# Optimization experiments

Measured on AMD Instinct MI355X. Metric: run time of the kernel, lower is better.

## Reference

```python
import jax, jax.numpy as jnp
import numpy as np

H = 4        # no_heads
CH = 32      # per-head hidden (c_hidden)
INF = 1.0e9

def setup_inputs() -> dict:
    key = jax.random.key(0)
    ks = jax.random.split(key, 8)
    B, I, J, C = 1, 256, 256, 128
    s = 0.02
    return {
        "x": jax.random.normal(ks[0], (B, I, J, C), jnp.float32),
        "mask": jnp.ones((B, I, J), jnp.float32),
        "chunk_size": 0,
        "ln_w": jnp.ones((C,), jnp.float32),
        "ln_b": jnp.zeros((C,), jnp.float32),
        "w_tri": jax.random.normal(ks[1], (C, H), jnp.float32) * s,
        "wq": jax.random.normal(ks[2], (C, H * CH), jnp.float32) * s,
        "wk": jax.random.normal(ks[3], (C, H * CH), jnp.float32) * s,
        "wv": jax.random.normal(ks[4], (C, H * CH), jnp.float32) * s,
        "wg": jax.random.normal(ks[5], (C, H * CH), jnp.float32) * s,
        "bg": jnp.zeros((H * CH,), jnp.float32),
        "wo": jax.random.normal(ks[6], (H * CH, C), jnp.float32) * s,
        "bo": jnp.zeros((C,), jnp.float32),
    }

def _layer_norm(x, w, b, eps=1e-5):
    mu = jnp.mean(x, axis=-1, keepdims=True)
    var = jnp.mean(jnp.square(x - mu), axis=-1, keepdims=True)
    return (x - mu) * jax.lax.rsqrt(var + eps) * w + b

def reference(x, mask, chunk_size, ln_w, ln_b, w_tri, wq, wk, wv, wg, bg, wo, bo):
    # starting=True -> no transpose of (I, J)
    B, I, J, C = x.shape
    xn = _layer_norm(x, ln_w, ln_b)                                   # [B,I,J,C]
    # biases
    mask_bias = (INF * (mask - 1.0))[:, :, None, None, :]             # [B,I,1,1,J]
    tri_bias = jnp.einsum("bijc,ch->bhij", xn, w_tri)[:, None]        # [B,1,H,I,J]
    # gated multi-head attention over the J axis (per row I)
    q = (xn @ wq).reshape(B, I, J, H, CH) * (CH ** -0.5)              # [B,I,J,H,CH]
    k = (xn @ wk).reshape(B, I, J, H, CH)
    v = (xn @ wv).reshape(B, I, J, H, CH)
    scores = jnp.einsum("biqhd,bikhd->bihqk", q, k) + mask_bias + tri_bias
    a = jax.nn.softmax(scores, axis=-1)                               # [B,I,H,J,J]
    o = jnp.einsum("bihqk,bikhd->biqhd", a, v)                        # [B,I,J,H,CH]
    g = jax.nn.sigmoid(xn @ wg + bg).reshape(B, I, J, H, CH)
    o = (o * g).reshape(B, I, J, H * CH)
    return o @ wo + bo                                                # [B,I,J,C]
```

## Files before the change

### kernel.cpp

```cpp
#include <hip/hip_runtime.h>
#include <math.h>

#define NI 256
#define NJ 256
#define NC 128
#define NH 4
#define NCH 32

typedef __attribute__((ext_vector_type(8)))  __bf16        bf16x8;
typedef __attribute__((ext_vector_type(8)))  unsigned short u16x8;
typedef __attribute__((ext_vector_type(4)))  unsigned int   u32x4;
typedef __attribute__((ext_vector_type(16))) float         f32x16;

__device__ __forceinline__ unsigned short f2bf(float f) {
    unsigned u = __builtin_bit_cast(unsigned, f);
    u += 0x7fffu + ((u >> 16) & 1u);
    return (unsigned short)(u >> 16);
}
__device__ __forceinline__ float bf2f(unsigned short s) {
    return __builtin_bit_cast(float, ((unsigned)s) << 16);
}
__device__ __forceinline__ f32x16 fzero16() {
    f32x16 z;
#pragma unroll
    for (int r = 0; r < 16; ++r) z[r] = 0.f;
    return z;
}
__device__ __forceinline__ f32x16 mfma16(bf16x8 a, bf16x8 b, f32x16 c) {
    return __builtin_amdgcn_mfma_f32_32x32x16_bf16(a, b, c, 0, 0, 0);
}

__global__ __launch_bounds__(256) void convert_weights(
    const float* __restrict__ wq, const float* __restrict__ wk,
    const float* __restrict__ wv, const float* __restrict__ wg,
    const float* __restrict__ wo, const float* __restrict__ w_tri,
    unsigned short* __restrict__ Wt_all, unsigned short* __restrict__ Wto,
    unsigned short* __restrict__ Wtri_pad)
{
    int id = blockIdx.x * 256 + threadIdx.x;
    if (id < 4 * 16384) {
        int m = id >> 14, r = id & 16383;
        int kk = r >> 7, c = r & 127;
        const float* W = (m == 0) ? wq : (m == 1) ? wk : (m == 2) ? wv : wg;
        Wt_all[(m * 128 + c) * 128 + kk] = f2bf(W[kk * 128 + c]);
    } else if (id < 5 * 16384) {
        int r = id - 4 * 16384;
        int kk = r >> 7, c = r & 127;
        Wto[c * 128 + kk] = f2bf(wo[kk * 128 + c]);
    } else {
        int r = id - 5 * 16384;
        int col = r >> 7, kk = r & 127;
        Wtri_pad[col * 128 + kk] = (col < NH) ? f2bf(w_tri[kk * NH + col]) : (unsigned short)0;
    }
}

#define XNP 136
__global__ __launch_bounds__(256, 2) void ln_proj_mfma(
    const float* __restrict__ x, const float* __restrict__ ln_w, const float* __restrict__ ln_b,
    const unsigned short* __restrict__ Wt_all, const unsigned short* __restrict__ Wtri_pad,
    const float* __restrict__ bg,
    unsigned short* __restrict__ q, unsigned short* __restrict__ k,
    unsigned short* __restrict__ v, unsigned short* __restrict__ g,
    float* __restrict__ tri)
{
    __shared__ unsigned short xn[64 * XNP];
    const int tid = threadIdx.x;
    const long tok0 = (long)blockIdx.x * 64;

    const int lane8 = tid & 7;
#pragma unroll
    for (int p = 0; p < 2; ++p) {
        const int t = p * 32 + (tid >> 3);
        const float4* xrow = (const float4*)(x + (tok0 + t) * NC + lane8 * 16);
        float4 xv[4];
        float s = 0.f;
#pragma unroll
        for (int u = 0; u < 4; ++u) {
            xv[u] = xrow[u];
            s += xv[u].x + xv[u].y + xv[u].z + xv[u].w;
        }
#pragma unroll
        for (int off = 4; off; off >>= 1) s += __shfl_down(s, off, 8);
        const float mu = __shfl(s, 0, 8) * (1.f / (float)NC);
        float s2 = 0.f;
#pragma unroll
        for (int u = 0; u < 4; ++u) {
            float dx;
            dx = xv[u].x - mu; s2 += dx * dx;
            dx = xv[u].y - mu; s2 += dx * dx;
            dx = xv[u].z - mu; s2 += dx * dx;
            dx = xv[u].w - mu; s2 += dx * dx;
        }
#pragma unroll
        for (int off = 4; off; off >>= 1) s2 += __shfl_down(s2, off, 8);
        const float rstd = rsqrtf(__shfl(s2, 0, 8) * (1.f / (float)NC) + 1e-5f);
#pragma unroll
        for (int u = 0; u < 4; ++u) {
            const int c = lane8 * 16 + u * 4;
            const float4 lw = *(const float4*)(ln_w + c);
            const float4 lb = *(const float4*)(ln_b + c);
            float o0 = (xv[u].x - mu) * rstd * lw.x + lb.x;
            float o1 = (xv[u].y - mu) * rstd * lw.y + lb.y;
            float o2 = (xv[u].z - mu) * rstd * lw.z + lb.z;
            float o3 = (xv[u].w - mu) * rstd * lw.w + lb.w;
            unsigned p0 = (unsigned)f2bf(o0) | ((unsigned)f2bf(o1) << 16);
            unsigned p1 = (unsigned)f2bf(o2) | ((unsigned)f2bf(o3) << 16);
            *(unsigned*)&xn[t * XNP + c]     = p0;
            *(unsigned*)&xn[t * XNP + c + 2] = p1;
        }
    }
    __syncthreads();

    const int w = tid >> 6, L = tid & 63, lh = L >> 5, lc = L & 31;
    f32x16 acc[2][4], accT[2];
#pragma unroll
    for (int mt = 0; mt < 2; ++mt) {
        accT[mt] = fzero16();
#pragma unroll
        for (int nt = 0; nt < 4; ++nt) acc[mt][nt] = fzero16();
    }

#pragma unroll
    for (int k0 = 0; k0 < 8; ++k0) {
        bf16x8 a0 = *(const bf16x8*)&xn[(lc)      * XNP + k0 * 16 + lh * 8];
        bf16x8 a1 = *(const bf16x8*)&xn[(32 + lc) * XNP + k0 * 16 + lh * 8];
#pragma unroll
        for (int nt = 0; nt < 4; ++nt) {
            const int ntile = w + 4 * nt;
            bf16x8 b = *(const bf16x8*)&Wt_all[(ntile * 32 + lc) * 128 + k0 * 16 + lh * 8];
            acc[0][nt] = mfma16(a0, b, acc[0][nt]);
            acc[1][nt] = mfma16(a1, b, acc[1][nt]);
        }
        bf16x8 bt = *(const bf16x8*)&Wtri_pad[lc * 128 + k0 * 16 + lh * 8];
        accT[0] = mfma16(a0, bt, accT[0]);
        accT[1] = mfma16(a1, bt, accT[1]);
    }

    const int a_row = (int)(tok0 >> 8);
    const int b0    = (int)(tok0 & 255);
    int rowl[16];
#pragma unroll
    for (int r = 0; r < 16; ++r) rowl[r] = (r & 3) + 8 * (r >> 2) + 4 * lh;

    const float bgv = bg[w * 32 + lc];
#pragma unroll
    for (int nt = 0; nt < 4; ++nt) {
        unsigned short* O = (nt == 0) ? q : (nt == 1) ? k : (nt == 2) ? v : g;
        unsigned short* Ob = O + (((long)a_row * NH + w) * NJ + b0) * NCH + lc;
#pragma unroll
        for (int mt = 0; mt < 2; ++mt) {
#pragma unroll
            for (int r = 0; r < 16; ++r) {
                const int row = mt * 32 + rowl[r];
                float val = acc[mt][nt][r];
                if (nt == 0) val *= 0.17677669529663689f;
                if (nt == 3) val = __builtin_amdgcn_rcpf(1.f + __expf(-(val + bgv)));
                Ob[(long)row * NCH] = f2bf(val);
            }
        }
    }
    if (lc < NH) {
        float* tb = tri + ((long)lc * NI + a_row) * NJ + b0;
#pragma unroll
        for (int mt = 0; mt < 2; ++mt)
#pragma unroll
            for (int r = 0; r < 16; ++r)
                tb[mt * 32 + rowl[r]] = accT[mt][r];
    }
}

#define LSP 260
__global__ __launch_bounds__(256) void swizzle_triT(
    const float* __restrict__ tri, float* __restrict__ tswz)
{
    __shared__ float Ls[32 * LSP];
    const int h = blockIdx.x, qt = blockIdx.y;
    const int tid = threadIdx.x;
#pragma unroll
    for (int it = 0; it < 8; ++it) {
        const int fi = it * 256 + tid;
        const int row = fi >> 6, c4 = fi & 63;
        *(float4*)&Ls[row * LSP + c4 * 4] =
            *(const float4*)(tri + ((long)h * NI + qt * 32 + row) * NJ + c4 * 4);
    }
    __syncthreads();
    const int kt = tid >> 5;
    const int lane2 = (tid & 31) * 2;
    float* dst = tswz + (((long)(h * 8 + qt) * 8 + kt) * 64 + lane2) * 16;
#pragma unroll
    for (int sub = 0; sub < 2; ++sub) {
        const int lane = lane2 + sub;
        const int lc = lane & 31, lhh = lane >> 5;
        float vals[16];
#pragma unroll
        for (int r = 0; r < 16; ++r)
            vals[r] = Ls[lc * LSP + kt * 32 + (r & 3) + 8 * (r >> 2) + 4 * lhh];
#pragma unroll
        for (int u = 0; u < 4; ++u)
            *(float4*)(dst + sub * 16 + u * 4) =
                make_float4(vals[4*u], vals[4*u+1], vals[4*u+2], vals[4*u+3]);
    }
}

#define KSP 40
#define VTP 264
#define GSP 40
#define OSP 36
__global__ __launch_bounds__(256, 2) void attn_fused(
    const unsigned short* __restrict__ q, const unsigned short* __restrict__ k,
    const unsigned short* __restrict__ v, const unsigned short* __restrict__ g,
    const float* __restrict__ tswz, const float* __restrict__ mask,
    const unsigned short* __restrict__ Wto, const float* __restrict__ bo,
    float* __restrict__ out)
{
    __shared__ char smem[48640];
    unsigned short* Ks = (unsigned short*)smem;
    unsigned short* Vt = (unsigned short*)(smem + 20480);
    unsigned short* Gs = (unsigned short*)(smem + 37376);
    float*       maskb = (float*)(smem + 47616);
    float*        outs = (float*)smem;

    const int i = blockIdx.x, qh = blockIdx.y;
    const int tid = threadIdx.x;
    const int w = tid >> 6, L = tid & 63, lh = L >> 5, lc = L & 31;
    const int qt = qh * 4 + w;
    const int qrow = qt * 32 + lc;

    maskb[tid] = 1.0e9f * (mask[i * NJ + tid] - 1.0f);

    f32x16 outacc[4];
#pragma unroll
    for (int ct = 0; ct < 4; ++ct) outacc[ct] = fzero16();

    for (int h = 0; h < NH; ++h) {
        if (h) __syncthreads();
        const long base = ((long)i * NH + h) * NJ * NCH;

#pragma unroll
        for (int it = 0; it < 4; ++it) {
            const int idx = it * 256 + tid;
            const int key = idx >> 2, c8 = (idx & 3) * 8;
            *(bf16x8*)&Ks[key * KSP + c8] = *(const bf16x8*)(k + base + key * NCH + c8);
        }
        {
            const int key = tid;
            const u16x8 r0 = *(const u16x8*)(v + base + key * NCH);
            const u16x8 r1 = *(const u16x8*)(v + base + key * NCH + 8);
            const u16x8 r2 = *(const u16x8*)(v + base + key * NCH + 16);
            const u16x8 r3 = *(const u16x8*)(v + base + key * NCH + 24);
#pragma unroll
            for (int u = 0; u < 8; ++u) {
                Vt[(u)      * VTP + key] = r0[u];
                Vt[(u + 8)  * VTP + key] = r1[u];
                Vt[(u + 16) * VTP + key] = r2[u];
                Vt[(u + 24) * VTP + key] = r3[u];
            }
        }
#pragma unroll
        for (int it = 0; it < 2; ++it) {
            const int idx = it * 256 + tid;
            const int row = idx >> 2, c8 = (idx & 3) * 8;
            *(bf16x8*)&Gs[row * GSP + c8] =
                *(const bf16x8*)(g + base + (qh * 128 + row) * NCH + c8);
        }
        __syncthreads();

        const bf16x8 a0 = *(const bf16x8*)(q + base + (long)qrow * NCH + lh * 8);
        const bf16x8 a1 = *(const bf16x8*)(q + base + (long)qrow * NCH + 16 + lh * 8);
        const float* tbase = tswz + ((long)(h * 8 + qt) * 8) * 1024 + (long)L * 16;

        float ls = 0.f;
        f32x16 O = fzero16();

#pragma unroll
        for (int t = 0; t < 8; ++t) {
            bf16x8 kb0 = *(const bf16x8*)&Ks[(t * 32 + lc) * KSP + lh * 8];
            bf16x8 kb1 = *(const bf16x8*)&Ks[(t * 32 + lc) * KSP + 16 + lh * 8];
            f32x16 s = fzero16();
            s = mfma16(kb0, a0, s);
            s = mfma16(kb1, a1, s);

            unsigned pk[8];
            const float* tv = tbase + (long)t * 1024;
#pragma unroll
            for (int gg = 0; gg < 4; ++gg) {
                const float4 tb = *(const float4*)(tv + gg * 4);
                const float4 mb = *(const float4*)&maskb[t * 32 + gg * 8 + 4 * lh];
                const float p0 = __expf(fminf(s[4 * gg + 0] + tb.x + mb.x, 30.f));
                const float p1 = __expf(fminf(s[4 * gg + 1] + tb.y + mb.y, 30.f));
                const float p2 = __expf(fminf(s[4 * gg + 2] + tb.z + mb.z, 30.f));
                const float p3 = __expf(fminf(s[4 * gg + 3] + tb.w + mb.w, 30.f));
                ls += (p0 + p1) + (p2 + p3);
                pk[2 * gg]     = (unsigned)f2bf(p0) | ((unsigned)f2bf(p1) << 16);
                pk[2 * gg + 1] = (unsigned)f2bf(p2) | ((unsigned)f2bf(p3) << 16);
            }

#pragma unroll
            for (int ss = 0; ss < 2; ++ss) {
                const unsigned give0 = lh ? pk[4 * ss]     : pk[4 * ss + 2];
                const unsigned give1 = lh ? pk[4 * ss + 1] : pk[4 * ss + 3];
                const unsigned t0 = __shfl_xor(give0, 32);
                const unsigned t1 = __shfl_xor(give1, 32);
                u32x4 bw;
                bw[0] = lh ? t0 : pk[4 * ss];
                bw[1] = lh ? t1 : pk[4 * ss + 1];
                bw[2] = lh ? pk[4 * ss + 2] : t0;
                bw[3] = lh ? pk[4 * ss + 3] : t1;
                const bf16x8 pb = __builtin_bit_cast(bf16x8, bw);
                const bf16x8 va = *(const bf16x8*)&Vt[lc * VTP + t * 32 + ss * 16 + lh * 8];
                O = mfma16(va, pb, O);
            }
        }

        ls += __shfl_xor(ls, 32);
        const float rl = __builtin_amdgcn_rcpf(ls);
        unsigned pk2[8];
#pragma unroll
        for (int gg = 0; gg < 4; ++gg) {
            const ushort4 gv = *(const ushort4*)&Gs[(w * 32 + lc) * GSP + gg * 8 + 4 * lh];
            const float o0 = O[4 * gg + 0] * rl * bf2f(gv.x);
            const float o1 = O[4 * gg + 1] * rl * bf2f(gv.y);
            const float o2 = O[4 * gg + 2] * rl * bf2f(gv.z);
            const float o3 = O[4 * gg + 3] * rl * bf2f(gv.w);
            pk2[2 * gg]     = (unsigned)f2bf(o0) | ((unsigned)f2bf(o1) << 16);
            pk2[2 * gg + 1] = (unsigned)f2bf(o2) | ((unsigned)f2bf(o3) << 16);
        }

#pragma unroll
        for (int ss = 0; ss < 2; ++ss) {
            const unsigned give0 = lh ? pk2[4 * ss]     : pk2[4 * ss + 2];
            const unsigned give1 = lh ? pk2[4 * ss + 1] : pk2[4 * ss + 3];
            const unsigned t0 = __shfl_xor(give0, 32);
            const unsigned t1 = __shfl_xor(give1, 32);
            u32x4 bw;
            bw[0] = lh ? t0 : pk2[4 * ss];
            bw[1] = lh ? t1 : pk2[4 * ss + 1];
            bw[2] = lh ? pk2[4 * ss + 2] : t0;
            bw[3] = lh ? pk2[4 * ss + 3] : t1;
            const bf16x8 ogb = __builtin_bit_cast(bf16x8, bw);
#pragma unroll
            for (int ct = 0; ct < 4; ++ct) {
                const bf16x8 wa = *(const bf16x8*)&Wto[(ct * 32 + lc) * 128 + h * 32 + ss * 16 + lh * 8];
                outacc[ct] = mfma16(wa, ogb, outacc[ct]);
            }
        }
    }

    int rowl[16];
#pragma unroll
    for (int r = 0; r < 16; ++r) rowl[r] = (r & 3) + 8 * (r >> 2) + 4 * lh;
#pragma unroll
    for (int ct = 0; ct < 4; ++ct) {
        __syncthreads();
#pragma unroll
        for (int r = 0; r < 16; ++r)
            outs[(w * 32 + lc) * OSP + rowl[r]] = outacc[ct][r];
        __syncthreads();
#pragma unroll
        for (int it = 0; it < 4; ++it) {
            const int fi = it * 256 + tid;
            const int row = fi >> 3, c4 = fi & 7;
            const float4 vv = *(const float4*)&outs[row * OSP + c4 * 4];
            const float4 bo4 = *(const float4*)(bo + ct * 32 + c4 * 4);
            float4 st;
            st.x = vv.x + bo4.x; st.y = vv.y + bo4.y;
            st.z = vv.z + bo4.z; st.w = vv.w + bo4.w;
            *(float4*)(out + ((long)i * NJ + qh * 128 + row) * NC + ct * 32 + c4 * 4) = st;
        }
    }
}

extern "C" void kernel_launch(void* const* d_in, const int* in_sizes, int n_in,
                              void* d_out, int out_size, void* d_ws, size_t ws_size,
                              hipStream_t stream) {
    const float* x     = (const float*)d_in[0];
    const float* mask  = (const float*)d_in[1];
    const float* ln_w  = (const float*)d_in[3];
    const float* ln_b  = (const float*)d_in[4];
    const float* w_tri = (const float*)d_in[5];
    const float* wq    = (const float*)d_in[6];
    const float* wk    = (const float*)d_in[7];
    const float* wv    = (const float*)d_in[8];
    const float* wg    = (const float*)d_in[9];
    const float* bg    = (const float*)d_in[10];
    const float* wo    = (const float*)d_in[11];
    const float* bo    = (const float*)d_in[12];
    float* out = (float*)d_out;

    char* p = (char*)d_ws;
    const long TOK = (long)NI * NJ;
    const long QB  = TOK * NC * sizeof(unsigned short);
    unsigned short* q  = (unsigned short*)p; p += QB;
    unsigned short* k  = (unsigned short*)p; p += QB;
    unsigned short* v  = (unsigned short*)p; p += QB;
    unsigned short* g  = (unsigned short*)p; p += QB;
    float* tri  = (float*)p; p += (long)NH * NI * NJ * sizeof(float);
    float* tswz = (float*)p; p += (long)NH * NI * NJ * sizeof(float);
    unsigned short* Wt_all   = (unsigned short*)p; p += 4 * 128 * 128 * sizeof(unsigned short);
    unsigned short* Wto      = (unsigned short*)p; p += 128 * 128 * sizeof(unsigned short);
    unsigned short* Wtri_pad = (unsigned short*)p; p += 32 * 128 * sizeof(unsigned short);

    hipLaunchKernelGGL(convert_weights, dim3(336), dim3(256), 0, stream,
                       wq, wk, wv, wg, wo, w_tri, Wt_all, Wto, Wtri_pad);
    hipLaunchKernelGGL(ln_proj_mfma, dim3(TOK / 64), dim3(256), 0, stream,
                       x, ln_w, ln_b, Wt_all, Wtri_pad, bg, q, k, v, g, tri);
    hipLaunchKernelGGL(swizzle_triT, dim3(NH, 8), dim3(256), 0, stream, tri, tswz);
    hipLaunchKernelGGL(attn_fused, dim3(NI, 2), dim3(256), 0, stream,
                       q, k, v, g, tswz, mask, Wto, bo, out);
}
```

Measured before the change: 179.8 us.

## Switch to fp16 MFMA, exp2 softmax, split keys across 8 waves, coalesce projection stores

Replaces bf16 with fp16 MFMA and round-toward-zero packing. Folds log2e into the scores, triangle bias and mask so softmax can use exp2, and loads the triangle bias straight into the accumulator. The attention kernel grows to 512 threads, with two waves per query tile each handling half the keys and merging partial results through LDS. The output projection is split across waves. The projection kernel stages outputs through LDS for vectorized stores, and the tri swizzle is retiled into smaller blocks. Trade-offs are fp16 range and precision and extra synchronization for the merge.

```diff
diff --git a/kernel.cpp b/kernel.cpp
--- a/kernel.cpp
+++ b/kernel.cpp
@@ -6,19 +6,18 @@
 #define NC 128
 #define NH 4
 #define NCH 32
-
-typedef __attribute__((ext_vector_type(8)))  __bf16        bf16x8;
-typedef __attribute__((ext_vector_type(8)))  unsigned short u16x8;
-typedef __attribute__((ext_vector_type(4)))  unsigned int   u32x4;
-typedef __attribute__((ext_vector_type(16))) float         f32x16;
-
-__device__ __forceinline__ unsigned short f2bf(float f) {
-    unsigned u = __builtin_bit_cast(unsigned, f);
-    u += 0x7fffu + ((u >> 16) & 1u);
-    return (unsigned short)(u >> 16);
-}
-__device__ __forceinline__ float bf2f(unsigned short s) {
-    return __builtin_bit_cast(float, ((unsigned)s) << 16);
+#define LOG2E 1.4426950408889634f
+
+typedef _Float16 f16x8 __attribute__((ext_vector_type(8)));
+typedef unsigned short u16x8 __attribute__((ext_vector_type(8)));
+typedef unsigned int u32x4 __attribute__((ext_vector_type(4)));
+typedef float f32x16 __attribute__((ext_vector_type(16)));
+
+__device__ __forceinline__ unsigned short f2h(float f) {
+    return __builtin_bit_cast(unsigned short, (_Float16)f);
+}
+__device__ __forceinline__ unsigned pkrtz(float a, float b) {
+    return __builtin_bit_cast(unsigned, __builtin_amdgcn_cvt_pkrtz(a, b));
 }
 __device__ __forceinline__ f32x16 fzero16() {
     f32x16 z;
@@ -26,8 +25,8 @@
     for (int r = 0; r < 16; ++r) z[r] = 0.f;
     return z;
 }
-__device__ __forceinline__ f32x16 mfma16(bf16x8 a, bf16x8 b, f32x16 c) {
-    return __builtin_amdgcn_mfma_f32_32x32x16_bf16(a, b, c, 0, 0, 0);
+__device__ __forceinline__ f32x16 mfma16f(f16x8 a, f16x8 b, f32x16 c) {
+    return __builtin_amdgcn_mfma_f32_32x32x16_f16(a, b, c, 0, 0, 0);
 }
 
 __global__ __launch_bounds__(256) void convert_weights(
@@ -42,15 +41,15 @@
         int m = id >> 14, r = id & 16383;
         int kk = r >> 7, c = r & 127;
         const float* W = (m == 0) ? wq : (m == 1) ? wk : (m == 2) ? wv : wg;
-        Wt_all[(m * 128 + c) * 128 + kk] = f2bf(W[kk * 128 + c]);
+        Wt_all[(m * 128 + c) * 128 + kk] = f2h(W[kk * 128 + c]);
     } else if (id < 5 * 16384) {
         int r = id - 4 * 16384;
         int kk = r >> 7, c = r & 127;
-        Wto[c * 128 + kk] = f2bf(wo[kk * 128 + c]);
+        Wto[c * 128 + kk] = f2h(wo[kk * 128 + c]);
     } else {
         int r = id - 5 * 16384;
         int col = r >> 7, kk = r & 127;
-        Wtri_pad[col * 128 + kk] = (col < NH) ? f2bf(w_tri[kk * NH + col]) : (unsigned short)0;
+        Wtri_pad[col * 128 + kk] = (col < NH) ? f2h(w_tri[kk * NH + col]) : (unsigned short)0;
     }
 }
 
@@ -103,10 +102,8 @@
             float o1 = (xv[u].y - mu) * rstd * lw.y + lb.y;
             float o2 = (xv[u].z - mu) * rstd * lw.z + lb.z;
             float o3 = (xv[u].w - mu) * rstd * lw.w + lb.w;
-            unsigned p0 = (unsigned)f2bf(o0) | ((unsigned)f2bf(o1) << 16);
-            unsigned p1 = (unsigned)f2bf(o2) | ((unsigned)f2bf(o3) << 16);
-            *(unsigned*)&xn[t * XNP + c]     = p0;
-            *(unsigned*)&xn[t * XNP + c + 2] = p1;
+            *(unsigned*)&xn[t * XNP + c]     = pkrtz(o0, o1);
+            *(unsigned*)&xn[t * XNP + c + 2] = pkrtz(o2, o3);
         }
     }
     __syncthreads();
@@ -122,18 +119,18 @@
 
 #pragma unroll
     for (int k0 = 0; k0 < 8; ++k0) {
-        bf16x8 a0 = *(const bf16x8*)&xn[(lc)      * XNP + k0 * 16 + lh * 8];
-        bf16x8 a1 = *(const bf16x8*)&xn[(32 + lc) * XNP + k0 * 16 + lh * 8];
+        f16x8 a0 = *(const f16x8*)&xn[(lc)      * XNP + k0 * 16 + lh * 8];
+        f16x8 a1 = *(const f16x8*)&xn[(32 + lc) * XNP + k0 * 16 + lh * 8];
 #pragma unroll
         for (int nt = 0; nt < 4; ++nt) {
             const int ntile = w + 4 * nt;
-            bf16x8 b = *(const bf16x8*)&Wt_all[(ntile * 32 + lc) * 128 + k0 * 16 + lh * 8];
-            acc[0][nt] = mfma16(a0, b, acc[0][nt]);
-            acc[1][nt] = mfma16(a1, b, acc[1][nt]);
-        }
-        bf16x8 bt = *(const bf16x8*)&Wtri_pad[lc * 128 + k0 * 16 + lh * 8];
-        accT[0] = mfma16(a0, bt, accT[0]);
-        accT[1] = mfma16(a1, bt, accT[1]);
+            f16x8 b = *(const f16x8*)&Wt_all[(ntile * 32 + lc) * 128 + k0 * 16 + lh * 8];
+            acc[0][nt] = mfma16f(a0, b, acc[0][nt]);
+            acc[1][nt] = mfma16f(a1, b, acc[1][nt]);
+        }
+        f16x8 bt = *(const f16x8*)&Wtri_pad[lc * 128 + k0 * 16 + lh * 8];
+        accT[0] = mfma16f(a0, bt, accT[0]);
+        accT[1] = mfma16f(a1, bt, accT[1]);
     }
 
     const int a_row = (int)(tok0 >> 8);
@@ -142,230 +139,261 @@
 #pragma unroll
     for (int r = 0; r < 16; ++r) rowl[r] = (r & 3) + 8 * (r >> 2) + 4 * lh;
 
+    if (lc < NH) {
+        float* tb = tri + ((long)lc * NI + a_row) * NJ + b0;
+#pragma unroll
+        for (int mt = 0; mt < 2; ++mt)
+#pragma unroll
+            for (int r = 0; r < 16; ++r)
+                tb[mt * 32 + rowl[r]] = accT[mt][r];
+    }
+
     const float bgv = bg[w * 32 + lc];
-#pragma unroll
-    for (int nt = 0; nt < 4; ++nt) {
-        unsigned short* O = (nt == 0) ? q : (nt == 1) ? k : (nt == 2) ? v : g;
-        unsigned short* Ob = O + (((long)a_row * NH + w) * NJ + b0) * NCH + lc;
+    const int token = tid >> 2, c8 = (tid & 3) * 8;
+#pragma unroll
+    for (int m = 0; m < 4; ++m) {
+        __syncthreads();
 #pragma unroll
         for (int mt = 0; mt < 2; ++mt) {
 #pragma unroll
             for (int r = 0; r < 16; ++r) {
                 const int row = mt * 32 + rowl[r];
-                float val = acc[mt][nt][r];
-                if (nt == 0) val *= 0.17677669529663689f;
-                if (nt == 3) val = __builtin_amdgcn_rcpf(1.f + __expf(-(val + bgv)));
-                Ob[(long)row * NCH] = f2bf(val);
-            }
-        }
-    }
-    if (lc < NH) {
-        float* tb = tri + ((long)lc * NI + a_row) * NJ + b0;
-#pragma unroll
-        for (int mt = 0; mt < 2; ++mt)
-#pragma unroll
-            for (int r = 0; r < 16; ++r)
-                tb[mt * 32 + rowl[r]] = accT[mt][r];
-    }
-}
-
-#define LSP 260
-__global__ __launch_bounds__(256) void swizzle_triT(
+                float val = acc[mt][m][r];
+                if (m == 0) val *= 0.25503486f;
+                if (m == 3) val = __builtin_amdgcn_rcpf(1.f + __builtin_amdgcn_exp2f(-LOG2E * (val + bgv)));
+                xn[row * XNP + w * 32 + lc] = f2h(val);
+            }
+        }
+        __syncthreads();
+        unsigned short* O = (m == 0) ? q : (m == 1) ? k : (m == 2) ? v : g;
+#pragma unroll
+        for (int hh = 0; hh < 4; ++hh) {
+            const u16x8 vec = *(const u16x8*)&xn[token * XNP + hh * 32 + c8];
+            *(u16x8*)(O + (((long)a_row * NH + hh) * NJ + b0 + token) * NCH + c8) = vec;
+        }
+    }
+}
+
+__global__ __launch_bounds__(64) void swizzle_triT(
     const float* __restrict__ tri, float* __restrict__ tswz)
 {
-    __shared__ float Ls[32 * LSP];
-    const int h = blockIdx.x, qt = blockIdx.y;
-    const int tid = threadIdx.x;
-#pragma unroll
-    for (int it = 0; it < 8; ++it) {
-        const int fi = it * 256 + tid;
-        const int row = fi >> 6, c4 = fi & 63;
-        *(float4*)&Ls[row * LSP + c4 * 4] =
-            *(const float4*)(tri + ((long)h * NI + qt * 32 + row) * NJ + c4 * 4);
+    __shared__ float Ls[32 * 36];
+    const int h = blockIdx.x, qt = blockIdx.y, kt = blockIdx.z;
+    const int l = threadIdx.x;
+#pragma unroll
+    for (int rr = 0; rr < 4; ++rr) {
+        const int fi = rr * 64 + l;
+        const int row = fi >> 3, c4 = fi & 7;
+        *(float4*)&Ls[row * 36 + c4 * 4] =
+            *(const float4*)(tri + ((long)h * NI + qt * 32 + row) * NJ + kt * 32 + c4 * 4);
     }
     __syncthreads();
-    const int kt = tid >> 5;
-    const int lane2 = (tid & 31) * 2;
-    float* dst = tswz + (((long)(h * 8 + qt) * 8 + kt) * 64 + lane2) * 16;
-#pragma unroll
-    for (int sub = 0; sub < 2; ++sub) {
-        const int lane = lane2 + sub;
-        const int lc = lane & 31, lhh = lane >> 5;
-        float vals[16];
-#pragma unroll
-        for (int r = 0; r < 16; ++r)
-            vals[r] = Ls[lc * LSP + kt * 32 + (r & 3) + 8 * (r >> 2) + 4 * lhh];
-#pragma unroll
-        for (int u = 0; u < 4; ++u)
-            *(float4*)(dst + sub * 16 + u * 4) =
-                make_float4(vals[4*u], vals[4*u+1], vals[4*u+2], vals[4*u+3]);
-    }
+    const int lc = l & 31, lhh = l >> 5;
+    float* dst = tswz + (((long)(h * 8 + qt) * 8 + kt) * 64 + l) * 16;
+    float vals[16];
+#pragma unroll
+    for (int r = 0; r < 16; ++r)
+        vals[r] = LOG2E * Ls[lc * 36 + kt * 0 + (r & 3) + 8 * (r >> 2) + 4 * lhh];
+#pragma unroll
+    for (int u = 0; u < 4; ++u)
+        *(float4*)(dst + u * 4) = make_float4(vals[4*u], vals[4*u+1], vals[4*u+2], vals[4*u+3]);
 }
 
 #define KSP 40
 #define VTP 264
+#define QSP 40
 #define GSP 40
-#define OSP 36
-__global__ __launch_bounds__(256, 2) void attn_fused(
+__global__ __launch_bounds__(512, 4) void attn_fused(
     const unsigned short* __restrict__ q, const unsigned short* __restrict__ k,
     const unsigned short* __restrict__ v, const unsigned short* __restrict__ g,
     const float* __restrict__ tswz, const float* __restrict__ mask,
     const unsigned short* __restrict__ Wto, const float* __restrict__ bo,
     float* __restrict__ out)
 {
-    __shared__ char smem[48640];
-    unsigned short* Ks = (unsigned short*)smem;
+    __shared__ char smem[79360];
+    unsigned short* Ks = (unsigned short*)(smem);
     unsigned short* Vt = (unsigned short*)(smem + 20480);
-    unsigned short* Gs = (unsigned short*)(smem + 37376);
-    float*       maskb = (float*)(smem + 47616);
-    float*        outs = (float*)smem;
+    unsigned short* Qs = (unsigned short*)(smem + 37376);
+    unsigned short* Gs = (unsigned short*)(smem + 47616);
+    float*       maskb = (float*)(smem + 57856);
+    float*         mrg = (float*)(smem + 58880);
 
     const int i = blockIdx.x, qh = blockIdx.y;
     const int tid = threadIdx.x;
     const int w = tid >> 6, L = tid & 63, lh = L >> 5, lc = L & 31;
-    const int qt = qh * 4 + w;
-    const int qrow = qt * 32 + lc;
-
-    maskb[tid] = 1.0e9f * (mask[i * NJ + tid] - 1.0f);
-
-    f32x16 outacc[4];
-#pragma unroll
-    for (int ct = 0; ct < 4; ++ct) outacc[ct] = fzero16();
+    const int wq4 = w & 3, ku = w >> 2;
+    const int qt = qh * 4 + wq4;
+    const int tb0 = ku * 4;
+
+    if (tid < 256) maskb[tid] = (LOG2E * 1.0e9f) * (mask[i * NJ + tid] - 1.0f);
+
+    int rowl[16];
+#pragma unroll
+    for (int r = 0; r < 16; ++r) rowl[r] = (r & 3) + 8 * (r >> 2) + 4 * lh;
+
+    f32x16 outacc[2];
+    outacc[0] = fzero16(); outacc[1] = fzero16();
+    float* myMrg = mrg + ((long)wq4 * 64 + L) * 20;
 
     for (int h = 0; h < NH; ++h) {
-        if (h) __syncthreads();
         const long base = ((long)i * NH + h) * NJ * NCH;
-
-#pragma unroll
-        for (int it = 0; it < 4; ++it) {
-            const int idx = it * 256 + tid;
+#pragma unroll
+        for (int it = 0; it < 2; ++it) {
+            const int idx = it * 512 + tid;
             const int key = idx >> 2, c8 = (idx & 3) * 8;
-            *(bf16x8*)&Ks[key * KSP + c8] = *(const bf16x8*)(k + base + key * NCH + c8);
+            *(u16x8*)&Ks[key * KSP + c8] = *(const u16x8*)(k + base + key * NCH + c8);
         }
         {
-            const int key = tid;
-            const u16x8 r0 = *(const u16x8*)(v + base + key * NCH);
-            const u16x8 r1 = *(const u16x8*)(v + base + key * NCH + 8);
-            const u16x8 r2 = *(const u16x8*)(v + base + key * NCH + 16);
-            const u16x8 r3 = *(const u16x8*)(v + base + key * NCH + 24);
+            const int row = tid >> 2, c8 = (tid & 3) * 8;
+            *(u16x8*)&Qs[row * QSP + c8] = *(const u16x8*)(q + base + (qh * 128 + row) * NCH + c8);
+            *(u16x8*)&Gs[row * GSP + c8] = *(const u16x8*)(g + base + (qh * 128 + row) * NCH + c8);
+        }
+        {
+            const int key = tid >> 1, hf = tid & 1;
+            const u16x8 r0 = *(const u16x8*)(v + base + key * NCH + hf * 16);
+            const u16x8 r1 = *(const u16x8*)(v + base + key * NCH + hf * 16 + 8);
 #pragma unroll
             for (int u = 0; u < 8; ++u) {
-                Vt[(u)      * VTP + key] = r0[u];
-                Vt[(u + 8)  * VTP + key] = r1[u];
-                Vt[(u + 16) * VTP + key] = r2[u];
-                Vt[(u + 24) * VTP + key] = r3[u];
-            }
-        }
-#pragma unroll
-        for (int it = 0; it < 2; ++it) {
-            const int idx = it * 256 + tid;
-            const int row = idx >> 2, c8 = (idx & 3) * 8;
-            *(bf16x8*)&Gs[row * GSP + c8] =
-                *(const bf16x8*)(g + base + (qh * 128 + row) * NCH + c8);
-        }
-        __syncthreads();
-
-        const bf16x8 a0 = *(const bf16x8*)(q + base + (long)qrow * NCH + lh * 8);
-        const bf16x8 a1 = *(const bf16x8*)(q + base + (long)qrow * NCH + 16 + lh * 8);
-        const float* tbase = tswz + ((long)(h * 8 + qt) * 8) * 1024 + (long)L * 16;
+                Vt[(hf * 16 + u)     * VTP + key] = r0[u];
+                Vt[(hf * 16 + 8 + u) * VTP + key] = r1[u];
+            }
+        }
+        __syncthreads();
+
+        const f16x8 a0 = *(const f16x8*)&Qs[(wq4 * 32 + lc) * QSP + lh * 8];
+        const f16x8 a1 = *(const f16x8*)&Qs[(wq4 * 32 + lc) * QSP + 16 + lh * 8];
 
         float ls = 0.f;
         f32x16 O = fzero16();
 
 #pragma unroll
-        for (int t = 0; t < 8; ++t) {
-            bf16x8 kb0 = *(const bf16x8*)&Ks[(t * 32 + lc) * KSP + lh * 8];
-            bf16x8 kb1 = *(const bf16x8*)&Ks[(t * 32 + lc) * KSP + 16 + lh * 8];
-            f32x16 s = fzero16();
-            s = mfma16(kb0, a0, s);
-            s = mfma16(kb1, a1, s);
+        for (int tt = 0; tt < 4; ++tt) {
+            const int t = tb0 + tt;
+            const float* tv = tswz + (((long)(h * 8 + qt)) * 8 + t) * 1024 + (long)L * 16;
+            f32x16 s;
+#pragma unroll
+            for (int u = 0; u < 4; ++u) {
+                const float4 t4 = *(const float4*)(tv + u * 4);
+                s[4*u] = t4.x; s[4*u+1] = t4.y; s[4*u+2] = t4.z; s[4*u+3] = t4.w;
+            }
+            const f16x8 kb0 = *(const f16x8*)&Ks[(t * 32 + lc) * KSP + lh * 8];
+            const f16x8 kb1 = *(const f16x8*)&Ks[(t * 32 + lc) * KSP + 16 + lh * 8];
+            s = mfma16f(kb0, a0, s);
+            s = mfma16f(kb1, a1, s);
 
             unsigned pk[8];
-            const float* tv = tbase + (long)t * 1024;
 #pragma unroll
             for (int gg = 0; gg < 4; ++gg) {
-                const float4 tb = *(const float4*)(tv + gg * 4);
                 const float4 mb = *(const float4*)&maskb[t * 32 + gg * 8 + 4 * lh];
-                const float p0 = __expf(fminf(s[4 * gg + 0] + tb.x + mb.x, 30.f));
-                const float p1 = __expf(fminf(s[4 * gg + 1] + tb.y + mb.y, 30.f));
-                const float p2 = __expf(fminf(s[4 * gg + 2] + tb.z + mb.z, 30.f));
-                const float p3 = __expf(fminf(s[4 * gg + 3] + tb.w + mb.w, 30.f));
+                const float p0 = __builtin_amdgcn_exp2f(fminf(s[4*gg+0] + mb.x, 15.f));
+                const float p1 = __builtin_amdgcn_exp2f(fminf(s[4*gg+1] + mb.y, 15.f));
+                const float p2 = __builtin_amdgcn_exp2f(fminf(s[4*gg+2] + mb.z, 15.f));
+                const float p3 = __builtin_amdgcn_exp2f(fminf(s[4*gg+3] + mb.w, 15.f));
                 ls += (p0 + p1) + (p2 + p3);
-                pk[2 * gg]     = (unsigned)f2bf(p0) | ((unsigned)f2bf(p1) << 16);
-                pk[2 * gg + 1] = (unsigned)f2bf(p2) | ((unsigned)f2bf(p3) << 16);
-            }
-
+                pk[2*gg]   = pkrtz(p0, p1);
+                pk[2*gg+1] = pkrtz(p2, p3);
+            }
 #pragma unroll
             for (int ss = 0; ss < 2; ++ss) {
-                const unsigned give0 = lh ? pk[4 * ss]     : pk[4 * ss + 2];
-                const unsigned give1 = lh ? pk[4 * ss + 1] : pk[4 * ss + 3];
+                const unsigned give0 = lh ? pk[4*ss]   : pk[4*ss+2];
+                const unsigned give1 = lh ? pk[4*ss+1] : pk[4*ss+3];
                 const unsigned t0 = __shfl_xor(give0, 32);
                 const unsigned t1 = __shfl_xor(give1, 32);
                 u32x4 bw;
-                bw[0] = lh ? t0 : pk[4 * ss];
-                bw[1] = lh ? t1 : pk[4 * ss + 1];
-                bw[2] = lh ? pk[4 * ss + 2] : t0;
-                bw[3] = lh ? pk[4 * ss + 3] : t1;
-                const bf16x8 pb = __builtin_bit_cast(bf16x8, bw);
-                const bf16x8 va = *(const bf16x8*)&Vt[lc * VTP + t * 32 + ss * 16 + lh * 8];
-                O = mfma16(va, pb, O);
-            }
-        }
-
-        ls += __shfl_xor(ls, 32);
-        const float rl = __builtin_amdgcn_rcpf(ls);
-        unsigned pk2[8];
-#pragma unroll
-        for (int gg = 0; gg < 4; ++gg) {
-            const ushort4 gv = *(const ushort4*)&Gs[(w * 32 + lc) * GSP + gg * 8 + 4 * lh];
-            const float o0 = O[4 * gg + 0] * rl * bf2f(gv.x);
-            const float o1 = O[4 * gg + 1] * rl * bf2f(gv.y);
-            const float o2 = O[4 * gg + 2] * rl * bf2f(gv.z);
-            const float o3 = O[4 * gg + 3] * rl * bf2f(gv.w);
-            pk2[2 * gg]     = (unsigned)f2bf(o0) | ((unsigned)f2bf(o1) << 16);
-            pk2[2 * gg + 1] = (unsigned)f2bf(o2) | ((unsigned)f2bf(o3) << 16);
-        }
-
-#pragma unroll
-        for (int ss = 0; ss < 2; ++ss) {
-            const unsigned give0 = lh ? pk2[4 * ss]     : pk2[4 * ss + 2];
-            const unsigned give1 = lh ? pk2[4 * ss + 1] : pk2[4 * ss + 3];
-            const unsigned t0 = __shfl_xor(give0, 32);
-            const unsigned t1 = __shfl_xor(give1, 32);
-            u32x4 bw;
-            bw[0] = lh ? t0 : pk2[4 * ss];
-            bw[1] = lh ? t1 : pk2[4 * ss + 1];
-            bw[2] = lh ? pk2[4 * ss + 2] : t0;
-            bw[3] = lh ? pk2[4 * ss + 3] : t1;
-            const bf16x8 ogb = __builtin_bit_cast(bf16x8, bw);
-#pragma unroll
-            for (int ct = 0; ct < 4; ++ct) {
-                const bf16x8 wa = *(const bf16x8*)&Wto[(ct * 32 + lc) * 128 + h * 32 + ss * 16 + lh * 8];
-                outacc[ct] = mfma16(wa, ogb, outacc[ct]);
-            }
-        }
-    }
-
-    int rowl[16];
-#pragma unroll
-    for (int r = 0; r < 16; ++r) rowl[r] = (r & 3) + 8 * (r >> 2) + 4 * lh;
-#pragma unroll
-    for (int ct = 0; ct < 4; ++ct) {
-        __syncthreads();
-#pragma unroll
-        for (int r = 0; r < 16; ++r)
-            outs[(w * 32 + lc) * OSP + rowl[r]] = outacc[ct][r];
+                bw[0] = lh ? t0 : pk[4*ss];
+                bw[1] = lh ? t1 : pk[4*ss+1];
+                bw[2] = lh ? pk[4*ss+2] : t0;
+                bw[3] = lh ? pk[4*ss+3] : t1;
+                const f16x8 pb = __builtin_bit_cast(f16x8, bw);
+                const f16x8 va = *(const f16x8*)&Vt[lc * VTP + t * 32 + ss * 16 + lh * 8];
+                O = mfma16f(va, pb, O);
+            }
+        }
+
+        if (ku) {
+#pragma unroll
+            for (int u = 0; u < 4; ++u)
+                *(float4*)(myMrg + u * 4) = make_float4(O[4*u], O[4*u+1], O[4*u+2], O[4*u+3]);
+            myMrg[16] = ls;
+        }
+        __syncthreads();
+        if (!ku) {
+#pragma unroll
+            for (int u = 0; u < 4; ++u) {
+                const float4 p4 = *(const float4*)(myMrg + u * 4);
+                O[4*u] += p4.x; O[4*u+1] += p4.y; O[4*u+2] += p4.z; O[4*u+3] += p4.w;
+            }
+            ls += myMrg[16];
+            ls += __shfl_xor(ls, 32);
+            const float rl = __builtin_amdgcn_rcpf(ls);
+            unsigned pg[8];
+#pragma unroll
+            for (int gg = 0; gg < 4; ++gg) {
+                const unsigned short* gp = &Gs[(wq4 * 32 + lc) * GSP + gg * 8 + 4 * lh];
+                const float o0 = O[4*gg+0] * rl * (float)*(const _Float16*)&gp[0];
+                const float o1 = O[4*gg+1] * rl * (float)*(const _Float16*)&gp[1];
+                const float o2 = O[4*gg+2] * rl * (float)*(const _Float16*)&gp[2];
+                const float o3 = O[4*gg+3] * rl * (float)*(const _Float16*)&gp[3];
+                pg[2*gg]   = pkrtz(o0, o1);
+                pg[2*gg+1] = pkrtz(o2, o3);
+            }
+            unsigned obw[8];
+#pragma unroll
+            for (int ss = 0; ss < 2; ++ss) {
+                const unsigned give0 = lh ? pg[4*ss]   : pg[4*ss+2];
+                const unsigned give1 = lh ? pg[4*ss+1] : pg[4*ss+3];
+                const unsigned t0 = __shfl_xor(give0, 32);
+                const unsigned t1 = __shfl_xor(give1, 32);
+                obw[4*ss+0] = lh ? t0 : pg[4*ss];
+                obw[4*ss+1] = lh ? t1 : pg[4*ss+1];
+                obw[4*ss+2] = lh ? pg[4*ss+2] : t0;
+                obw[4*ss+3] = lh ? pg[4*ss+3] : t1;
+            }
+            u32x4 w0, w1;
+#pragma unroll
+            for (int u = 0; u < 4; ++u) { w0[u] = obw[u]; w1[u] = obw[4+u]; }
+            ((u32x4*)myMrg)[0] = w0;
+            ((u32x4*)myMrg)[1] = w1;
+        }
+        __syncthreads();
+        {
+            const u32x4 b0v = ((const u32x4*)myMrg)[0];
+            const u32x4 b1v = ((const u32x4*)myMrg)[1];
+#pragma unroll
+            for (int ss = 0; ss < 2; ++ss) {
+                const f16x8 ogf = __builtin_bit_cast(f16x8, ss ? b1v : b0v);
+#pragma unroll
+                for (int c2 = 0; c2 < 2; ++c2) {
+                    const f16x8 wa = *(const f16x8*)(Wto + ((ku * 2 + c2) * 32 + lc) * NC
+                                                     + h * NCH + ss * 16 + lh * 8);
+                    outacc[c2] = mfma16f(wa, ogf, outacc[c2]);
+                }
+            }
+        }
+    }
+
+    float* outs = (float*)smem;
+#pragma unroll
+    for (int ph = 0; ph < 2; ++ph) {
+        __syncthreads();
+        if (ku == ph) {
+#pragma unroll
+            for (int c2 = 0; c2 < 2; ++c2)
+#pragma unroll
+                for (int r = 0; r < 16; ++r)
+                    outs[(wq4 * 32 + lc) * 68 + c2 * 32 + rowl[r]] = outacc[c2][r];
+        }
         __syncthreads();
 #pragma unroll
         for (int it = 0; it < 4; ++it) {
-            const int fi = it * 256 + tid;
-            const int row = fi >> 3, c4 = fi & 7;
-            const float4 vv = *(const float4*)&outs[row * OSP + c4 * 4];
-            const float4 bo4 = *(const float4*)(bo + ct * 32 + c4 * 4);
+            const int fi = it * 512 + tid;
+            const int qrow = fi >> 4, c4 = fi & 15;
+            const float4 vv = *(const float4*)&outs[qrow * 68 + c4 * 4];
+            const float4 b4 = *(const float4*)(bo + ph * 64 + c4 * 4);
             float4 st;
-            st.x = vv.x + bo4.x; st.y = vv.y + bo4.y;
-            st.z = vv.z + bo4.z; st.w = vv.w + bo4.w;
-            *(float4*)(out + ((long)i * NJ + qh * 128 + row) * NC + ct * 32 + c4 * 4) = st;
+            st.x = vv.x + b4.x; st.y = vv.y + b4.y;
+            st.z = vv.z + b4.z; st.w = vv.w + b4.w;
+            *(float4*)(out + ((long)i * NJ + qh * 128 + qrow) * NC + ph * 64 + c4 * 4) = st;
         }
     }
 }
@@ -404,7 +432,7 @@
                        wq, wk, wv, wg, wo, w_tri, Wt_all, Wto, Wtri_pad);
     hipLaunchKernelGGL(ln_proj_mfma, dim3(TOK / 64), dim3(256), 0, stream,
                        x, ln_w, ln_b, Wt_all, Wtri_pad, bg, q, k, v, g, tri);
-    hipLaunchKernelGGL(swizzle_triT, dim3(NH, 8), dim3(256), 0, stream, tri, tswz);
-    hipLaunchKernelGGL(attn_fused, dim3(NI, 2), dim3(256), 0, stream,
+    hipLaunchKernelGGL(swizzle_triT, dim3(NH, 8, 8), dim3(64), 0, stream, tri, tswz);
+    hipLaunchKernelGGL(attn_fused, dim3(NI, 2), dim3(512), 0, stream,
                        q, k, v, g, tswz, mask, Wto, bo, out);
 }
```

After: 181.4 us. Within noise of the previous version (+0.9%).
